# Kernel tuning notes

Hardware: AMD Instinct MI355X
Metric: run time of the kernel (lower is better)

The kernel has to match this reference:

```python
import jax, jax.numpy as jnp
import numpy as np

B, N, D = 4, 4096, 512
H = 8
HD = D // H  # 64


def setup_inputs() -> dict:
    key = jax.random.key(0)
    ks = jax.random.split(key, 9)
    s = 1.0 / np.sqrt(D)
    return {
        "x": jax.random.normal(ks[0], (B, N, D), dtype=jnp.float32),
        "Wq": jax.random.normal(ks[1], (D, D), dtype=jnp.float32) * s,
        "bq": jax.random.normal(ks[2], (D,), dtype=jnp.float32) * 0.01,
        "Wk": jax.random.normal(ks[3], (D, D), dtype=jnp.float32) * s,
        "bk": jax.random.normal(ks[4], (D,), dtype=jnp.float32) * 0.01,
        "Wv": jax.random.normal(ks[5], (D, D), dtype=jnp.float32) * s,
        "bv": jax.random.normal(ks[6], (D,), dtype=jnp.float32) * 0.01,
        "Wo": jax.random.normal(ks[7], (D, D), dtype=jnp.float32) * s,
        "bo": jax.random.normal(ks[8], (D,), dtype=jnp.float32) * 0.01,
    }


def reference(x, Wq, bq, Wk, bk, Wv, bv, Wo, bo):
    # projections -> [B, H, N, HD]
    def split_heads(t):
        return t.reshape(B, N, H, HD).transpose(0, 2, 1, 3)

    q = split_heads(x @ Wq.T + bq)
    k = split_heads(x @ Wk.T + bk)
    v = split_heads(x @ Wv.T + bv)

    scale = 1.0 / np.sqrt(HD).astype(np.float32)
    scores = jnp.einsum("bhqd,bhkd->bhqk", q, k) * scale  # [B,H,N,N]
    attn = jax.nn.softmax(scores, axis=-1)
    out = jnp.einsum("bhqk,bhkd->bhqd", attn, v)  # [B,H,N,HD]
    out = out.transpose(0, 2, 1, 3).reshape(B, N, D)
    return out @ Wo.T + bo
```

## Files before the change

### kernel.cpp

```cpp
#include <hip/hip_runtime.h>
#include <hip/hip_bf16.h>

#define BB 4
#define NN 4096
#define DD 512
#define HH 8
#define HD 64

typedef __attribute__((ext_vector_type(4))) float f32x4;
typedef __attribute__((ext_vector_type(16))) float f32x16;
typedef __attribute__((ext_vector_type(8))) short short8;
typedef __attribute__((ext_vector_type(4))) unsigned int uint4v;

static __device__ __forceinline__ unsigned short f2bf(float f) {
    unsigned int u = __float_as_uint(f);
    u += 0x7fff + ((u >> 16) & 1);
    return (unsigned short)(u >> 16);
}

__global__ void convert_bf16(const float* __restrict__ in,
                             unsigned short* __restrict__ out, int n) {
    int i = (blockIdx.x * blockDim.x + threadIdx.x) * 8;
    int stride = gridDim.x * blockDim.x * 8;
    for (; i + 7 < n; i += stride) {
        f32x4 a = *reinterpret_cast<const f32x4*>(in + i);
        f32x4 b = *reinterpret_cast<const f32x4*>(in + i + 4);
        short8 o;
        o[0] = (short)f2bf(a[0]); o[1] = (short)f2bf(a[1]);
        o[2] = (short)f2bf(a[2]); o[3] = (short)f2bf(a[3]);
        o[4] = (short)f2bf(b[0]); o[5] = (short)f2bf(b[1]);
        o[6] = (short)f2bf(b[2]); o[7] = (short)f2bf(b[3]);
        *reinterpret_cast<short8*>(out + i) = o;
    }
}

__global__ void convert_weights(const float* __restrict__ W0, const float* __restrict__ W1,
                                const float* __restrict__ W2, const float* __restrict__ W3,
                                unsigned short* __restrict__ out) {
    int which = blockIdx.x >> 7;
    const float* src = which == 0 ? W0 : which == 1 ? W1 : which == 2 ? W2 : W3;
    unsigned short* dst = out + (size_t)which * DD * DD;
    int i = ((blockIdx.x & 127) * blockDim.x + threadIdx.x) * 8;
    f32x4 a = *reinterpret_cast<const f32x4*>(src + i);
    f32x4 b = *reinterpret_cast<const f32x4*>(src + i + 4);
    short8 o;
    o[0] = (short)f2bf(a[0]); o[1] = (short)f2bf(a[1]);
    o[2] = (short)f2bf(a[2]); o[3] = (short)f2bf(a[3]);
    o[4] = (short)f2bf(b[0]); o[5] = (short)f2bf(b[1]);
    o[6] = (short)f2bf(b[2]); o[7] = (short)f2bf(b[3]);
    *reinterpret_cast<short8*>(dst + i) = o;
}

template <int OUT_BF16>
__global__ __launch_bounds__(256)
void gemm_bias(const unsigned short* __restrict__ A,
               const unsigned short* __restrict__ W,
               const float* __restrict__ bias,
               void* __restrict__ Cout, float scale) {
    __shared__ uint4 ldsA[128 * 4];
    __shared__ uint4 ldsB[128 * 4];
    const int t = threadIdx.x;
    const int lane = t & 63;
    const int w = t >> 6;
    const int wr = w >> 1, wc = w & 1;
    const int brow = (int)blockIdx.y * 128;
    const int bcol = (int)blockIdx.x * 128;
    const int l16 = lane & 15;
    const int lq = lane >> 4;

    f32x4 acc[4][4] = {};

    const int sr = t >> 1;
    const int c16 = (t & 1) * 2;

    for (int k0 = 0; k0 < 512; k0 += 32) {
        const uint4* gA = reinterpret_cast<const uint4*>(A + (size_t)(brow + sr) * 512 + k0 + c16 * 8);
        const uint4* gB = reinterpret_cast<const uint4*>(W + (size_t)(bcol + sr) * 512 + k0 + c16 * 8);
        uint4 a0 = gA[0], a1 = gA[1];
        uint4 b0 = gB[0], b1 = gB[1];
        __syncthreads();
        ldsA[(sr * 4 + c16) ^ (sr & 7)]     = a0;
        ldsA[(sr * 4 + c16 + 1) ^ (sr & 7)] = a1;
        ldsB[(sr * 4 + c16) ^ (sr & 7)]     = b0;
        ldsB[(sr * 4 + c16 + 1) ^ (sr & 7)] = b1;
        __syncthreads();
        short8 af[4], bfr[4];
#pragma unroll
        for (int m = 0; m < 4; ++m) {
            int ra = wr * 64 + m * 16 + l16;
            af[m] = *reinterpret_cast<short8*>(&ldsA[(ra * 4 + lq) ^ (ra & 7)]);
            int rb = wc * 64 + m * 16 + l16;
            bfr[m] = *reinterpret_cast<short8*>(&ldsB[(rb * 4 + lq) ^ (rb & 7)]);
        }
#pragma unroll
        for (int m = 0; m < 4; ++m)
#pragma unroll
            for (int n = 0; n < 4; ++n)
                acc[m][n] = __builtin_amdgcn_mfma_f32_16x16x32_bf16(af[m], bfr[n], acc[m][n], 0, 0, 0);
    }

#pragma unroll
    for (int m = 0; m < 4; ++m) {
        int row = brow + wr * 64 + m * 16 + lq * 4;
#pragma unroll
        for (int n = 0; n < 4; ++n) {
            int col = bcol + wc * 64 + n * 16 + l16;
            float bv = bias[col];
#pragma unroll
            for (int r = 0; r < 4; ++r) {
                float v = (acc[m][n][r] + bv) * scale;
                if (OUT_BF16) {
                    ((unsigned short*)Cout)[(size_t)(row + r) * 512 + col] = f2bf(v);
                } else {
                    ((float*)Cout)[(size_t)(row + r) * 512 + col] = v;
                }
            }
        }
    }
}

__global__ __launch_bounds__(256)
void transpose_v(const unsigned short* __restrict__ Vb, unsigned short* __restrict__ Vt) {
    __shared__ unsigned short tile[64][72];
    const int bh = blockIdx.y;
    const int b = bh >> 3, h = bh & 7;
    const int n0 = blockIdx.x * 64;
    const int t = threadIdx.x;
    {
        int r = t >> 2;
        int cs = (t & 3) * 16;
        const short8* src = reinterpret_cast<const short8*>(
            Vb + (size_t)(b * NN + n0 + r) * DD + h * HD + cs);
        short8 v0 = src[0], v1 = src[1];
#pragma unroll
        for (int j = 0; j < 8; ++j) {
            tile[r][cs + j]     = (unsigned short)v0[j];
            tile[r][cs + 8 + j] = (unsigned short)v1[j];
        }
    }
    __syncthreads();
    {
        int d = t >> 2;
        int ns = (t & 3) * 16;
        short8 o0, o1;
#pragma unroll
        for (int j = 0; j < 8; ++j) {
            o0[j] = (short)tile[ns + j][d];
            o1[j] = (short)tile[ns + 8 + j][d];
        }
        unsigned short* dst = Vt + ((size_t)bh * HD + d) * NN + n0 + ns;
        *reinterpret_cast<short8*>(dst)     = o0;
        *reinterpret_cast<short8*>(dst + 8) = o1;
    }
}

__global__ __launch_bounds__(256)
void flash_attn(const unsigned short* __restrict__ Qb,
                const unsigned short* __restrict__ Kb,
                const unsigned short* __restrict__ Vt,
                unsigned short* __restrict__ Ob) {
    __shared__ __align__(16) char lds[32768];
    const int t = threadIdx.x;
    const int lane = t & 63;
    const int w = t >> 6;
    const int nid = (blockIdx.x & 7) * 128 + (blockIdx.x >> 3);
    const int bh = nid >> 5;
    const int qb = nid & 31;
    const int b = bh >> 3, h = bh & 7;
    const int q0 = qb * 128 + w * 32;
    const int l32 = lane & 31;
    const int hi = lane >> 5;

    const int i8 = lane >> 3, g8 = lane & 7;

    const unsigned short* qptr = Qb + (size_t)(b * NN + q0 + l32) * DD + h * HD + hi * 8;
    short8 qf[4];
#pragma unroll
    for (int c = 0; c < 4; ++c)
        qf[c] = *reinterpret_cast<const short8*>(qptr + c * 16);

    const f32x16 Z = {};
    f32x16 OT0 = {}, OT1 = {};
    float lsum = 0.f;

    int koff[8], voff[8];
#pragma unroll
    for (int sub = 0; sub < 2; ++sub) {
#pragma unroll
        for (int c = 0; c < 4; ++c) {
            int row = sub * 32 + l32;
            int g = (hi + 2 * c) ^ (row & 7) ^ ((row >> 3) & 7);
            koff[sub * 4 + c] = row * 128 + g * 16;
        }
#pragma unroll
        for (int dblk = 0; dblk < 2; ++dblk)
#pragma unroll
            for (int c2 = 0; c2 < 2; ++c2) {
                int row = dblk * 32 + l32;
                int g = ((sub << 2) + (c2 << 1) + hi) ^ (row & 7) ^ ((row >> 3) & 7);
                voff[sub * 4 + dblk * 2 + c2] = 8192 + row * 128 + g * 16;
            }
    }

    const int rowl0 = w * 16 + i8;
    const int rowl1 = w * 16 + 8 + i8;
    const int gs0 = (g8 ^ i8 ^ ((2 * w) & 7)) * 8;
    const int gs1 = (g8 ^ i8 ^ ((2 * w + 1) & 7)) * 8;
    const unsigned short* kp0 = Kb + (size_t)(b * NN + rowl0) * DD + h * HD + gs0;
    const unsigned short* kp1 = Kb + (size_t)(b * NN + rowl1) * DD + h * HD + gs1;
    const unsigned short* vp0 = Vt + ((size_t)bh * HD + rowl0) * NN + gs0;
    const unsigned short* vp1 = Vt + ((size_t)bh * HD + rowl1) * NN + gs1;

    auto STAGE = [&](int bb) {
        __builtin_amdgcn_global_load_lds(
            (const __attribute__((address_space(1))) void*)kp0,
            (__attribute__((address_space(3))) void*)(lds + bb + (w * 16) * 128), 16, 0, 0);
        __builtin_amdgcn_global_load_lds(
            (const __attribute__((address_space(1))) void*)kp1,
            (__attribute__((address_space(3))) void*)(lds + bb + (w * 16 + 8) * 128), 16, 0, 0);
        __builtin_amdgcn_global_load_lds(
            (const __attribute__((address_space(1))) void*)vp0,
            (__attribute__((address_space(3))) void*)(lds + bb + 8192 + (w * 16) * 128), 16, 0, 0);
        __builtin_amdgcn_global_load_lds(
            (const __attribute__((address_space(1))) void*)vp1,
            (__attribute__((address_space(3))) void*)(lds + bb + 8192 + (w * 16 + 8) * 128), 16, 0, 0);
        kp0 += 64 * DD; kp1 += 64 * DD; vp0 += 64; vp1 += 64;
    };

    auto softpack = [&](const f32x16& S, short8& pa, short8& pb) {
        unsigned int wq[8];
#pragma unroll
        for (int j = 0; j < 8; ++j) {
            float p0 = __builtin_exp2f(S[2 * j]);
            float p1 = __builtin_exp2f(S[2 * j + 1]);
            lsum += p0 + p1;
            asm("v_cvt_pk_bf16_f32 %0, %1, %2" : "=v"(wq[j]) : "v"(p0), "v"(p1));
        }
        asm("v_permlane32_swap_b32 %0, %1" : "+v"(wq[0]), "+v"(wq[2]));
        asm("v_permlane32_swap_b32 %0, %1" : "+v"(wq[1]), "+v"(wq[3]));
        asm("v_permlane32_swap_b32 %0, %1" : "+v"(wq[4]), "+v"(wq[6]));
        asm("v_permlane32_swap_b32 %0, %1" : "+v"(wq[5]), "+v"(wq[7]));
        uint4v pu0 = {wq[0], wq[1], wq[2], wq[3]};
        uint4v pu1 = {wq[4], wq[5], wq[6], wq[7]};
        pa = __builtin_bit_cast(short8, pu0);
        pb = __builtin_bit_cast(short8, pu1);
    };

    auto COMPUTE = [&](int BO) {
        short8 kf[8];
#pragma unroll
        for (int i = 0; i < 8; ++i)
            kf[i] = *reinterpret_cast<const short8*>(lds + BO + koff[i]);

        f32x16 S0, S1;
        S0 = __builtin_amdgcn_mfma_f32_32x32x16_bf16(kf[0], qf[0], Z, 0, 0, 0);
        S1 = __builtin_amdgcn_mfma_f32_32x32x16_bf16(kf[4], qf[0], Z, 0, 0, 0);
        S0 = __builtin_amdgcn_mfma_f32_32x32x16_bf16(kf[1], qf[1], S0, 0, 0, 0);
        S1 = __builtin_amdgcn_mfma_f32_32x32x16_bf16(kf[5], qf[1], S1, 0, 0, 0);
        S0 = __builtin_amdgcn_mfma_f32_32x32x16_bf16(kf[2], qf[2], S0, 0, 0, 0);
        S1 = __builtin_amdgcn_mfma_f32_32x32x16_bf16(kf[6], qf[2], S1, 0, 0, 0);
        S0 = __builtin_amdgcn_mfma_f32_32x32x16_bf16(kf[3], qf[3], S0, 0, 0, 0);
        S1 = __builtin_amdgcn_mfma_f32_32x32x16_bf16(kf[7], qf[3], S1, 0, 0, 0);

        short8 vf[8];
#pragma unroll
        for (int i = 0; i < 8; ++i)
            vf[i] = *reinterpret_cast<const short8*>(lds + BO + voff[i]);

        short8 p0a, p0b, p1a, p1b;
        softpack(S0, p0a, p0b);
        OT0 = __builtin_amdgcn_mfma_f32_32x32x16_bf16(vf[0], p0a, OT0, 0, 0, 0);
        OT0 = __builtin_amdgcn_mfma_f32_32x32x16_bf16(vf[1], p0b, OT0, 0, 0, 0);
        OT1 = __builtin_amdgcn_mfma_f32_32x32x16_bf16(vf[2], p0a, OT1, 0, 0, 0);
        OT1 = __builtin_amdgcn_mfma_f32_32x32x16_bf16(vf[3], p0b, OT1, 0, 0, 0);
        softpack(S1, p1a, p1b);
        OT0 = __builtin_amdgcn_mfma_f32_32x32x16_bf16(vf[4], p1a, OT0, 0, 0, 0);
        OT0 = __builtin_amdgcn_mfma_f32_32x32x16_bf16(vf[5], p1b, OT0, 0, 0, 0);
        OT1 = __builtin_amdgcn_mfma_f32_32x32x16_bf16(vf[6], p1a, OT1, 0, 0, 0);
        OT1 = __builtin_amdgcn_mfma_f32_32x32x16_bf16(vf[7], p1b, OT1, 0, 0, 0);
    };

    STAGE(0);
    asm volatile("s_waitcnt vmcnt(0)" ::: "memory");
    __builtin_amdgcn_s_barrier();
    asm volatile("" ::: "memory");

    for (int it = 0; it < 32; ++it) {
        STAGE(16384);
        asm volatile("s_waitcnt vmcnt(4)" ::: "memory");
        __builtin_amdgcn_s_barrier();
        asm volatile("" ::: "memory");
        COMPUTE(0);
        asm volatile("" ::: "memory");
        __builtin_amdgcn_s_barrier();
        asm volatile("" ::: "memory");
        if (it != 31) {
            STAGE(0);
            asm volatile("s_waitcnt vmcnt(4)" ::: "memory");
        } else {
            asm volatile("s_waitcnt vmcnt(0)" ::: "memory");
        }
        __builtin_amdgcn_s_barrier();
        asm volatile("" ::: "memory");
        COMPUTE(16384);
        if (it != 31) {
            asm volatile("" ::: "memory");
            __builtin_amdgcn_s_barrier();
            asm volatile("" ::: "memory");
        }
    }

    lsum += __shfl_xor(lsum, 32);
    float inv = 1.0f / lsum;
    char* lw = lds + w * 4096;
#pragma unroll
    for (int dblk = 0; dblk < 2; ++dblk) {
#pragma unroll
        for (int g = 0; g < 4; ++g) {
#pragma unroll
            for (int j = 0; j < 2; ++j) {
                int r = 4 * g + 2 * j;
                int d = dblk * 32 + 8 * g + 2 * j + 4 * hi;
                float a = (dblk ? OT1[r] : OT0[r]) * inv;
                float bqv = (dblk ? OT1[r + 1] : OT0[r + 1]) * inv;
                unsigned int wv;
                asm("v_cvt_pk_bf16_f32 %0, %1, %2" : "=v"(wv) : "v"(a), "v"(bqv));
                int addr = (l32 * 128 + d * 2) ^ ((l32 & 7) << 4);
                *reinterpret_cast<unsigned int*>(lw + addr) = wv;
            }
        }
    }
#pragma unroll
    for (int it = 0; it < 4; ++it) {
        int q = lane >> 1;
        int seg = (lane & 1) + it * 2;
        uint4 val = *reinterpret_cast<uint4*>(lw + ((q * 128 + seg * 16) ^ ((q & 7) << 4)));
        *reinterpret_cast<uint4*>(Ob + (size_t)(b * NN + q0 + q) * DD + h * HD + seg * 8) = val;
    }
}

extern "C" void kernel_launch(void* const* d_in, const int* in_sizes, int n_in,
                              void* d_out, int out_size, void* d_ws, size_t ws_size,
                              hipStream_t stream) {
    (void)in_sizes; (void)n_in; (void)out_size; (void)ws_size;
    const float* x  = (const float*)d_in[0];
    const float* Wq = (const float*)d_in[1];
    const float* bq = (const float*)d_in[2];
    const float* Wk = (const float*)d_in[3];
    const float* bk = (const float*)d_in[4];
    const float* Wv = (const float*)d_in[5];
    const float* bv = (const float*)d_in[6];
    const float* Wo = (const float*)d_in[7];
    const float* bo = (const float*)d_in[8];
    float* out = (float*)d_out;

    char* ws = (char*)d_ws;
    const size_t BUF = 16777216;
    unsigned short* xb  = (unsigned short*)(ws);
    unsigned short* Qb  = (unsigned short*)(ws + BUF);
    unsigned short* Kb  = (unsigned short*)(ws + 2 * BUF);
    unsigned short* Vb  = (unsigned short*)(ws + 3 * BUF);
    unsigned short* Wqb = (unsigned short*)(ws + 4 * BUF);
    unsigned short* Wkb = Wqb + 262144;
    unsigned short* Wvb = Wkb + 262144;
    unsigned short* Wob = Wvb + 262144;
    unsigned short* Vt  = xb;
    unsigned short* Ob  = Vb;

    const int NTOK = BB * NN;
    const float cl = 0.125f * 1.4426950408889634f;

    convert_bf16<<<2048, 256, 0, stream>>>(x, xb, NTOK * DD);
    convert_weights<<<512, 256, 0, stream>>>(Wq, Wk, Wv, Wo, Wqb);

    dim3 ggrid(4, NTOK / 128);
    gemm_bias<1><<<ggrid, 256, 0, stream>>>(xb, Wqb, bq, Qb, cl);
    gemm_bias<1><<<ggrid, 256, 0, stream>>>(xb, Wkb, bk, Kb, 1.0f);
    gemm_bias<1><<<ggrid, 256, 0, stream>>>(xb, Wvb, bv, Vb, 1.0f);

    transpose_v<<<dim3(NN / 64, BB * HH), 256, 0, stream>>>(Vb, Vt);

    flash_attn<<<1024, 256, 0, stream>>>(Qb, Kb, Vt, Ob);

    gemm_bias<0><<<ggrid, 256, 0, stream>>>(Ob, Wob, bo, out, 1.0f);
}
```

Baseline: 297.5 us.

## Restructure flash-attn double-buffer pipeline with early LDS reads, setprio, occupancy hint

The K/V main loop is rebuilt so each phase waits for its buffer, loads all K and V fragments from LDS into registers, and barriers. It then immediately issues the global-to-LDS stage for the next tile into the same buffer, so the copy overlaps the MFMA and softmax work. Both buffers are prefetched before the loop. The MFMA sequences are wrapped in s_setprio to favour matrix issue, and launch_bounds requests 4 blocks per CU. The risks are higher register pressure from holding kf and vf together, a possible spill under the occupancy hint, and the correctness of the new vmcnt(4) wait accounting.

```diff
diff --git a/kernel.cpp b/kernel.cpp
--- a/kernel.cpp
+++ b/kernel.cpp
@@ -154,7 +154,7 @@
     }
 }
 
-__global__ __launch_bounds__(256)
+__global__ __launch_bounds__(256, 4)
 void flash_attn(const unsigned short* __restrict__ Qb,
                 const unsigned short* __restrict__ Kb,
                 const unsigned short* __restrict__ Vt,
@@ -246,13 +246,25 @@
         pb = __builtin_bit_cast(short8, pu1);
     };
 
-    auto COMPUTE = [&](int BO) {
-        short8 kf[8];
+    auto PHASE = [&](int BO, bool doStage, bool lastDrain) {
+        if (lastDrain) asm volatile("s_waitcnt vmcnt(0)" ::: "memory");
+        else           asm volatile("s_waitcnt vmcnt(4)" ::: "memory");
+        __builtin_amdgcn_s_barrier();
+        asm volatile("" ::: "memory");
+        short8 kf[8], vf[8];
 #pragma unroll
         for (int i = 0; i < 8; ++i)
             kf[i] = *reinterpret_cast<const short8*>(lds + BO + koff[i]);
+#pragma unroll
+        for (int i = 0; i < 8; ++i)
+            vf[i] = *reinterpret_cast<const short8*>(lds + BO + voff[i]);
+        asm volatile("s_waitcnt lgkmcnt(0)" ::: "memory");
+        __builtin_amdgcn_s_barrier();
+        asm volatile("" ::: "memory");
+        if (doStage) STAGE(BO);
 
         f32x16 S0, S1;
+        __builtin_amdgcn_s_setprio(1);
         S0 = __builtin_amdgcn_mfma_f32_32x32x16_bf16(kf[0], qf[0], Z, 0, 0, 0);
         S1 = __builtin_amdgcn_mfma_f32_32x32x16_bf16(kf[4], qf[0], Z, 0, 0, 0);
         S0 = __builtin_amdgcn_mfma_f32_32x32x16_bf16(kf[1], qf[1], S0, 0, 0, 0);
@@ -261,53 +273,31 @@
         S1 = __builtin_amdgcn_mfma_f32_32x32x16_bf16(kf[6], qf[2], S1, 0, 0, 0);
         S0 = __builtin_amdgcn_mfma_f32_32x32x16_bf16(kf[3], qf[3], S0, 0, 0, 0);
         S1 = __builtin_amdgcn_mfma_f32_32x32x16_bf16(kf[7], qf[3], S1, 0, 0, 0);
-
-        short8 vf[8];
-#pragma unroll
-        for (int i = 0; i < 8; ++i)
-            vf[i] = *reinterpret_cast<const short8*>(lds + BO + voff[i]);
+        __builtin_amdgcn_s_setprio(0);
 
         short8 p0a, p0b, p1a, p1b;
         softpack(S0, p0a, p0b);
+        __builtin_amdgcn_s_setprio(1);
         OT0 = __builtin_amdgcn_mfma_f32_32x32x16_bf16(vf[0], p0a, OT0, 0, 0, 0);
         OT0 = __builtin_amdgcn_mfma_f32_32x32x16_bf16(vf[1], p0b, OT0, 0, 0, 0);
         OT1 = __builtin_amdgcn_mfma_f32_32x32x16_bf16(vf[2], p0a, OT1, 0, 0, 0);
         OT1 = __builtin_amdgcn_mfma_f32_32x32x16_bf16(vf[3], p0b, OT1, 0, 0, 0);
+        __builtin_amdgcn_s_setprio(0);
         softpack(S1, p1a, p1b);
+        __builtin_amdgcn_s_setprio(1);
         OT0 = __builtin_amdgcn_mfma_f32_32x32x16_bf16(vf[4], p1a, OT0, 0, 0, 0);
         OT0 = __builtin_amdgcn_mfma_f32_32x32x16_bf16(vf[5], p1b, OT0, 0, 0, 0);
         OT1 = __builtin_amdgcn_mfma_f32_32x32x16_bf16(vf[6], p1a, OT1, 0, 0, 0);
         OT1 = __builtin_amdgcn_mfma_f32_32x32x16_bf16(vf[7], p1b, OT1, 0, 0, 0);
+        __builtin_amdgcn_s_setprio(0);
     };
 
     STAGE(0);
-    asm volatile("s_waitcnt vmcnt(0)" ::: "memory");
-    __builtin_amdgcn_s_barrier();
-    asm volatile("" ::: "memory");
+    STAGE(16384);
 
     for (int it = 0; it < 32; ++it) {
-        STAGE(16384);
-        asm volatile("s_waitcnt vmcnt(4)" ::: "memory");
-        __builtin_amdgcn_s_barrier();
-        asm volatile("" ::: "memory");
-        COMPUTE(0);
-        asm volatile("" ::: "memory");
-        __builtin_amdgcn_s_barrier();
-        asm volatile("" ::: "memory");
-        if (it != 31) {
-            STAGE(0);
-            asm volatile("s_waitcnt vmcnt(4)" ::: "memory");
-        } else {
-            asm volatile("s_waitcnt vmcnt(0)" ::: "memory");
-        }
-        __builtin_amdgcn_s_barrier();
-        asm volatile("" ::: "memory");
-        COMPUTE(16384);
-        if (it != 31) {
-            asm volatile("" ::: "memory");
-            __builtin_amdgcn_s_barrier();
-            asm volatile("" ::: "memory");
-        }
+        PHASE(0,     it < 31, false);
+        PHASE(16384, it < 31, it == 31);
     }
 
     lsum += __shfl_xor(lsum, 32);
```

New measurement: 688.5 us. +131.4%, slower.

## Software-pipeline QK and PV MFMAs with fewer live registers and setprio

Applied to the files above, without the earlier changes.

Restructures the per-tile compute so that the second QK^T block's MFMAs interleave with the first PV block's MFMAs. K and V fragments are loaded in halves, which cuts live VGPRs, and launch bounds are raised to target 3 waves-per-SIMD occupancy. It also adds s_setprio around MFMA groups and splits the row-sum accumulator into two independent chains. The aim is to overlap softmax exp and LDS reads with matrix-core work and to raise occupancy. The risks are register spills under the tighter bound and serialisation on the reused S accumulator.

```diff
diff --git a/kernel.cpp b/kernel.cpp
--- a/kernel.cpp
+++ b/kernel.cpp
@@ -154,7 +154,7 @@
     }
 }
 
-__global__ __launch_bounds__(256)
+__global__ __launch_bounds__(256, 3)
 void flash_attn(const unsigned short* __restrict__ Qb,
                 const unsigned short* __restrict__ Kb,
                 const unsigned short* __restrict__ Vt,
@@ -181,7 +181,7 @@
 
     const f32x16 Z = {};
     f32x16 OT0 = {}, OT1 = {};
-    float lsum = 0.f;
+    float lsx = 0.f, lsy = 0.f;
 
     int koff[8], voff[8];
 #pragma unroll
@@ -233,7 +233,7 @@
         for (int j = 0; j < 8; ++j) {
             float p0 = __builtin_exp2f(S[2 * j]);
             float p1 = __builtin_exp2f(S[2 * j + 1]);
-            lsum += p0 + p1;
+            lsx += p0; lsy += p1;
             asm("v_cvt_pk_bf16_f32 %0, %1, %2" : "=v"(wq[j]) : "v"(p0), "v"(p1));
         }
         asm("v_permlane32_swap_b32 %0, %1" : "+v"(wq[0]), "+v"(wq[2]));
@@ -247,37 +247,49 @@
     };
 
     auto COMPUTE = [&](int BO) {
-        short8 kf[8];
-#pragma unroll
-        for (int i = 0; i < 8; ++i)
-            kf[i] = *reinterpret_cast<const short8*>(lds + BO + koff[i]);
-
-        f32x16 S0, S1;
-        S0 = __builtin_amdgcn_mfma_f32_32x32x16_bf16(kf[0], qf[0], Z, 0, 0, 0);
-        S1 = __builtin_amdgcn_mfma_f32_32x32x16_bf16(kf[4], qf[0], Z, 0, 0, 0);
-        S0 = __builtin_amdgcn_mfma_f32_32x32x16_bf16(kf[1], qf[1], S0, 0, 0, 0);
-        S1 = __builtin_amdgcn_mfma_f32_32x32x16_bf16(kf[5], qf[1], S1, 0, 0, 0);
-        S0 = __builtin_amdgcn_mfma_f32_32x32x16_bf16(kf[2], qf[2], S0, 0, 0, 0);
-        S1 = __builtin_amdgcn_mfma_f32_32x32x16_bf16(kf[6], qf[2], S1, 0, 0, 0);
-        S0 = __builtin_amdgcn_mfma_f32_32x32x16_bf16(kf[3], qf[3], S0, 0, 0, 0);
-        S1 = __builtin_amdgcn_mfma_f32_32x32x16_bf16(kf[7], qf[3], S1, 0, 0, 0);
-
-        short8 vf[8];
-#pragma unroll
-        for (int i = 0; i < 8; ++i)
-            vf[i] = *reinterpret_cast<const short8*>(lds + BO + voff[i]);
-
-        short8 p0a, p0b, p1a, p1b;
-        softpack(S0, p0a, p0b);
-        OT0 = __builtin_amdgcn_mfma_f32_32x32x16_bf16(vf[0], p0a, OT0, 0, 0, 0);
-        OT0 = __builtin_amdgcn_mfma_f32_32x32x16_bf16(vf[1], p0b, OT0, 0, 0, 0);
-        OT1 = __builtin_amdgcn_mfma_f32_32x32x16_bf16(vf[2], p0a, OT1, 0, 0, 0);
-        OT1 = __builtin_amdgcn_mfma_f32_32x32x16_bf16(vf[3], p0b, OT1, 0, 0, 0);
-        softpack(S1, p1a, p1b);
-        OT0 = __builtin_amdgcn_mfma_f32_32x32x16_bf16(vf[4], p1a, OT0, 0, 0, 0);
-        OT0 = __builtin_amdgcn_mfma_f32_32x32x16_bf16(vf[5], p1b, OT0, 0, 0, 0);
-        OT1 = __builtin_amdgcn_mfma_f32_32x32x16_bf16(vf[6], p1a, OT1, 0, 0, 0);
-        OT1 = __builtin_amdgcn_mfma_f32_32x32x16_bf16(vf[7], p1b, OT1, 0, 0, 0);
+        short8 kf0, kf1, kf2, kf3;
+        kf0 = *reinterpret_cast<const short8*>(lds + BO + koff[0]);
+        kf1 = *reinterpret_cast<const short8*>(lds + BO + koff[1]);
+        kf2 = *reinterpret_cast<const short8*>(lds + BO + koff[2]);
+        kf3 = *reinterpret_cast<const short8*>(lds + BO + koff[3]);
+        f32x16 S;
+        __builtin_amdgcn_s_setprio(1);
+        S = __builtin_amdgcn_mfma_f32_32x32x16_bf16(kf0, qf[0], Z, 0, 0, 0);
+        S = __builtin_amdgcn_mfma_f32_32x32x16_bf16(kf1, qf[1], S, 0, 0, 0);
+        S = __builtin_amdgcn_mfma_f32_32x32x16_bf16(kf2, qf[2], S, 0, 0, 0);
+        S = __builtin_amdgcn_mfma_f32_32x32x16_bf16(kf3, qf[3], S, 0, 0, 0);
+        __builtin_amdgcn_s_setprio(0);
+        short8 vf0 = *reinterpret_cast<const short8*>(lds + BO + voff[0]);
+        short8 vf1 = *reinterpret_cast<const short8*>(lds + BO + voff[1]);
+        short8 vf2 = *reinterpret_cast<const short8*>(lds + BO + voff[2]);
+        short8 vf3 = *reinterpret_cast<const short8*>(lds + BO + voff[3]);
+        kf0 = *reinterpret_cast<const short8*>(lds + BO + koff[4]);
+        kf1 = *reinterpret_cast<const short8*>(lds + BO + koff[5]);
+        kf2 = *reinterpret_cast<const short8*>(lds + BO + koff[6]);
+        kf3 = *reinterpret_cast<const short8*>(lds + BO + koff[7]);
+        short8 pa, pb;
+        softpack(S, pa, pb);
+        __builtin_amdgcn_s_setprio(1);
+        S = __builtin_amdgcn_mfma_f32_32x32x16_bf16(kf0, qf[0], Z, 0, 0, 0);
+        S = __builtin_amdgcn_mfma_f32_32x32x16_bf16(kf1, qf[1], S, 0, 0, 0);
+        OT0 = __builtin_amdgcn_mfma_f32_32x32x16_bf16(vf0, pa, OT0, 0, 0, 0);
+        OT0 = __builtin_amdgcn_mfma_f32_32x32x16_bf16(vf1, pb, OT0, 0, 0, 0);
+        S = __builtin_amdgcn_mfma_f32_32x32x16_bf16(kf2, qf[2], S, 0, 0, 0);
+        S = __builtin_amdgcn_mfma_f32_32x32x16_bf16(kf3, qf[3], S, 0, 0, 0);
+        OT1 = __builtin_amdgcn_mfma_f32_32x32x16_bf16(vf2, pa, OT1, 0, 0, 0);
+        OT1 = __builtin_amdgcn_mfma_f32_32x32x16_bf16(vf3, pb, OT1, 0, 0, 0);
+        __builtin_amdgcn_s_setprio(0);
+        vf0 = *reinterpret_cast<const short8*>(lds + BO + voff[4]);
+        vf1 = *reinterpret_cast<const short8*>(lds + BO + voff[5]);
+        vf2 = *reinterpret_cast<const short8*>(lds + BO + voff[6]);
+        vf3 = *reinterpret_cast<const short8*>(lds + BO + voff[7]);
+        softpack(S, pa, pb);
+        __builtin_amdgcn_s_setprio(1);
+        OT0 = __builtin_amdgcn_mfma_f32_32x32x16_bf16(vf0, pa, OT0, 0, 0, 0);
+        OT0 = __builtin_amdgcn_mfma_f32_32x32x16_bf16(vf1, pb, OT0, 0, 0, 0);
+        OT1 = __builtin_amdgcn_mfma_f32_32x32x16_bf16(vf2, pa, OT1, 0, 0, 0);
+        OT1 = __builtin_amdgcn_mfma_f32_32x32x16_bf16(vf3, pb, OT1, 0, 0, 0);
+        __builtin_amdgcn_s_setprio(0);
     };
 
     STAGE(0);
@@ -310,6 +322,7 @@
         }
     }
 
+    float lsum = lsx + lsy;
     lsum += __shfl_xor(lsum, 32);
     float inv = 1.0f / lsum;
     char* lw = lds + w * 4096;
```

Result: slower. 335.7 us (+12.8%).

## Fuse QKV GEMMs into one launch and widen flash-attn blocks to 8 waves

Applied to the files above, without the earlier changes.

Merges the three Q/K/V projection GEMMs into a single launch indexed by grid z. Flash attention now uses 512-thread blocks covering 256 queries, so each staged K/V tile in LDS is shared by 8 waves instead of 4, halving per-query K/V global loads. The row-sum accumulation is split into two accumulators to shorten the dependency chain. The trade-off is barriers across 8 waves and fewer, larger blocks.

```diff
diff --git a/kernel.cpp b/kernel.cpp
--- a/kernel.cpp
+++ b/kernel.cpp
@@ -52,19 +52,16 @@
 }
 
 template <int OUT_BF16>
-__global__ __launch_bounds__(256)
-void gemm_bias(const unsigned short* __restrict__ A,
+__device__ __forceinline__
+void gemm_tile(const unsigned short* __restrict__ A,
                const unsigned short* __restrict__ W,
                const float* __restrict__ bias,
-               void* __restrict__ Cout, float scale) {
-    __shared__ uint4 ldsA[128 * 4];
-    __shared__ uint4 ldsB[128 * 4];
+               void* __restrict__ Cout, float scale,
+               int brow, int bcol, uint4* ldsA, uint4* ldsB) {
     const int t = threadIdx.x;
     const int lane = t & 63;
     const int w = t >> 6;
     const int wr = w >> 1, wc = w & 1;
-    const int brow = (int)blockIdx.y * 128;
-    const int bcol = (int)blockIdx.x * 128;
     const int l16 = lane & 15;
     const int lq = lane >> 4;
 
@@ -117,6 +114,35 @@
             }
         }
     }
+}
+
+__global__ __launch_bounds__(256)
+void gemm_qkv(const unsigned short* __restrict__ xb,
+              const unsigned short* __restrict__ Wall,
+              const float* __restrict__ bq, const float* __restrict__ bk,
+              const float* __restrict__ bv,
+              unsigned short* __restrict__ Qb, unsigned short* __restrict__ Kb,
+              unsigned short* __restrict__ Vb, float cl) {
+    __shared__ uint4 ldsA[128 * 4];
+    __shared__ uint4 ldsB[128 * 4];
+    int z = blockIdx.z;
+    const unsigned short* W = Wall + (size_t)z * DD * DD;
+    const float* bias = z == 0 ? bq : z == 1 ? bk : bv;
+    unsigned short* dst = z == 0 ? Qb : z == 1 ? Kb : Vb;
+    float scale = z == 0 ? cl : 1.0f;
+    gemm_tile<1>(xb, W, bias, dst, scale,
+                 (int)blockIdx.y * 128, (int)blockIdx.x * 128, ldsA, ldsB);
+}
+
+__global__ __launch_bounds__(256)
+void gemm_bias_f32(const unsigned short* __restrict__ A,
+                   const unsigned short* __restrict__ W,
+                   const float* __restrict__ bias,
+                   float* __restrict__ Cout) {
+    __shared__ uint4 ldsA[128 * 4];
+    __shared__ uint4 ldsB[128 * 4];
+    gemm_tile<0>(A, W, bias, Cout, 1.0f,
+                 (int)blockIdx.y * 128, (int)blockIdx.x * 128, ldsA, ldsB);
 }
 
 __global__ __launch_bounds__(256)
@@ -154,7 +180,7 @@
     }
 }
 
-__global__ __launch_bounds__(256)
+__global__ __launch_bounds__(512)
 void flash_attn(const unsigned short* __restrict__ Qb,
                 const unsigned short* __restrict__ Kb,
                 const unsigned short* __restrict__ Vt,
@@ -163,11 +189,11 @@
     const int t = threadIdx.x;
     const int lane = t & 63;
     const int w = t >> 6;
-    const int nid = (blockIdx.x & 7) * 128 + (blockIdx.x >> 3);
-    const int bh = nid >> 5;
-    const int qb = nid & 31;
+    const int nid = (blockIdx.x & 7) * 64 + (blockIdx.x >> 3);
+    const int bh = nid >> 4;
+    const int qb = nid & 15;
     const int b = bh >> 3, h = bh & 7;
-    const int q0 = qb * 128 + w * 32;
+    const int q0 = qb * 256 + w * 32;
     const int l32 = lane & 31;
     const int hi = lane >> 5;
 
@@ -181,7 +207,7 @@
 
     const f32x16 Z = {};
     f32x16 OT0 = {}, OT1 = {};
-    float lsum = 0.f;
+    float lsx = 0.f, lsy = 0.f;
 
     int koff[8], voff[8];
 #pragma unroll
@@ -202,29 +228,19 @@
             }
     }
 
-    const int rowl0 = w * 16 + i8;
-    const int rowl1 = w * 16 + 8 + i8;
-    const int gs0 = (g8 ^ i8 ^ ((2 * w) & 7)) * 8;
-    const int gs1 = (g8 ^ i8 ^ ((2 * w + 1) & 7)) * 8;
-    const unsigned short* kp0 = Kb + (size_t)(b * NN + rowl0) * DD + h * HD + gs0;
-    const unsigned short* kp1 = Kb + (size_t)(b * NN + rowl1) * DD + h * HD + gs1;
-    const unsigned short* vp0 = Vt + ((size_t)bh * HD + rowl0) * NN + gs0;
-    const unsigned short* vp1 = Vt + ((size_t)bh * HD + rowl1) * NN + gs1;
+    const int rowl = w * 8 + i8;
+    const int gsw = (g8 ^ i8 ^ (w & 7)) * 8;
+    const unsigned short* kp = Kb + (size_t)(b * NN + rowl) * DD + h * HD + gsw;
+    const unsigned short* vp = Vt + ((size_t)bh * HD + rowl) * NN + gsw;
 
     auto STAGE = [&](int bb) {
         __builtin_amdgcn_global_load_lds(
-            (const __attribute__((address_space(1))) void*)kp0,
-            (__attribute__((address_space(3))) void*)(lds + bb + (w * 16) * 128), 16, 0, 0);
+            (const __attribute__((address_space(1))) void*)kp,
+            (__attribute__((address_space(3))) void*)(lds + bb + w * 1024), 16, 0, 0);
         __builtin_amdgcn_global_load_lds(
-            (const __attribute__((address_space(1))) void*)kp1,
-            (__attribute__((address_space(3))) void*)(lds + bb + (w * 16 + 8) * 128), 16, 0, 0);
-        __builtin_amdgcn_global_load_lds(
-            (const __attribute__((address_space(1))) void*)vp0,
-            (__attribute__((address_space(3))) void*)(lds + bb + 8192 + (w * 16) * 128), 16, 0, 0);
-        __builtin_amdgcn_global_load_lds(
-            (const __attribute__((address_space(1))) void*)vp1,
-            (__attribute__((address_space(3))) void*)(lds + bb + 8192 + (w * 16 + 8) * 128), 16, 0, 0);
-        kp0 += 64 * DD; kp1 += 64 * DD; vp0 += 64; vp1 += 64;
+            (const __attribute__((address_space(1))) void*)vp,
+            (__attribute__((address_space(3))) void*)(lds + bb + 8192 + w * 1024), 16, 0, 0);
+        kp += 64 * DD; vp += 64;
     };
 
     auto softpack = [&](const f32x16& S, short8& pa, short8& pb) {
@@ -233,7 +249,7 @@
         for (int j = 0; j < 8; ++j) {
             float p0 = __builtin_exp2f(S[2 * j]);
             float p1 = __builtin_exp2f(S[2 * j + 1]);
-            lsum += p0 + p1;
+            lsx += p0; lsy += p1;
             asm("v_cvt_pk_bf16_f32 %0, %1, %2" : "=v"(wq[j]) : "v"(p0), "v"(p1));
         }
         asm("v_permlane32_swap_b32 %0, %1" : "+v"(wq[0]), "+v"(wq[2]));
@@ -287,7 +303,7 @@
 
     for (int it = 0; it < 32; ++it) {
         STAGE(16384);
-        asm volatile("s_waitcnt vmcnt(4)" ::: "memory");
+        asm volatile("s_waitcnt vmcnt(2)" ::: "memory");
         __builtin_amdgcn_s_barrier();
         asm volatile("" ::: "memory");
         COMPUTE(0);
@@ -296,7 +312,7 @@
         asm volatile("" ::: "memory");
         if (it != 31) {
             STAGE(0);
-            asm volatile("s_waitcnt vmcnt(4)" ::: "memory");
+            asm volatile("s_waitcnt vmcnt(2)" ::: "memory");
         } else {
             asm volatile("s_waitcnt vmcnt(0)" ::: "memory");
         }
@@ -310,6 +326,7 @@
         }
     }
 
+    float lsum = lsx + lsy;
     lsum += __shfl_xor(lsum, 32);
     float inv = 1.0f / lsum;
     char* lw = lds + w * 4096;
@@ -361,9 +378,7 @@
     unsigned short* Kb  = (unsigned short*)(ws + 2 * BUF);
     unsigned short* Vb  = (unsigned short*)(ws + 3 * BUF);
     unsigned short* Wqb = (unsigned short*)(ws + 4 * BUF);
-    unsigned short* Wkb = Wqb + 262144;
-    unsigned short* Wvb = Wkb + 262144;
-    unsigned short* Wob = Wvb + 262144;
+    unsigned short* Wob = Wqb + 3 * 262144;
     unsigned short* Vt  = xb;
     unsigned short* Ob  = Vb;
 
@@ -373,14 +388,12 @@
     convert_bf16<<<2048, 256, 0, stream>>>(x, xb, NTOK * DD);
     convert_weights<<<512, 256, 0, stream>>>(Wq, Wk, Wv, Wo, Wqb);
 
-    dim3 ggrid(4, NTOK / 128);
-    gemm_bias<1><<<ggrid, 256, 0, stream>>>(xb, Wqb, bq, Qb, cl);
-    gemm_bias<1><<<ggrid, 256, 0, stream>>>(xb, Wkb, bk, Kb, 1.0f);
-    gemm_bias<1><<<ggrid, 256, 0, stream>>>(xb, Wvb, bv, Vb, 1.0f);
+    dim3 ggrid(4, NTOK / 128, 3);
+    gemm_qkv<<<ggrid, 256, 0, stream>>>(xb, Wqb, bq, bk, bv, Qb, Kb, Vb, cl);
 
     transpose_v<<<dim3(NN / 64, BB * HH), 256, 0, stream>>>(Vb, Vt);
 
-    flash_attn<<<1024, 256, 0, stream>>>(Qb, Kb, Vt, Ob);
-
-    gemm_bias<0><<<ggrid, 256, 0, stream>>>(Ob, Wob, bo, out, 1.0f);
-}
+    flash_attn<<<512, 512, 0, stream>>>(Qb, Kb, Vt, Ob);
+
+    gemm_bias_f32<<<dim3(4, NTOK / 128), 256, 0, stream>>>(Ob, Wob, bo, out);
+}
```

Measured after the change: 274.8 us. -7.6%, faster.
